# Performance work log

Hardware: AMD Instinct MI355X
Metric: run time of the kernel (lower is better)

The kernel has to match this reference:

```python
import jax, jax.numpy as jnp
import numpy as np
from jax import lax

N, R, W, H = 256, 32, 8, 6       # batch, n_rooms, room width/height
MX, MY = 72, 72                  # map grid
EMB = 6                          # room embedding width
CIN = 10 + EMB                   # conv input channels


def _boundaries(m):
    # m: [R, W, H] binary room masks -> [R, 4, W, H] (left, right, up, down edges)
    left = jnp.concatenate([m[:, :1, :], jnp.clip(m[:, 1:, :] - m[:, :-1, :], 0)], axis=1)
    right = jnp.concatenate([jnp.clip(m[:, :-1, :] - m[:, 1:, :], 0), m[:, -1:, :]], axis=1)
    up = jnp.concatenate([m[:, :, :1], jnp.clip(m[:, :, 1:] - m[:, :, :-1], 0)], axis=2)
    down = jnp.concatenate([jnp.clip(m[:, :, :-1] - m[:, :, 1:], 0), m[:, :, -1:]], axis=2)
    return jnp.stack([left, right, up, down], axis=1)


def setup_inputs() -> dict:
    key = jax.random.key(0)
    ks = jax.random.split(key, 12)
    room_map = (jax.random.uniform(ks[0], (R, W, H)) < 0.7).astype(jnp.float32)
    room_map = room_map.at[:, 0, 0].set(1.0)  # guarantee nonempty rooms
    doors = (jax.random.uniform(ks[1], (R, 4, W, H)) < 0.15).astype(jnp.float32) * room_map[:, None]
    room_tensor = jnp.concatenate([room_map[:, None], doors, _boundaries(room_map)], axis=1)  # [R,9,W,H]
    px = jax.random.randint(ks[2], (N, R), 0, MX - W)
    py = jax.random.randint(ks[3], (N, R), 0, MY - H)
    room_positions = jnp.stack([px, py], axis=-1).astype(jnp.int32)  # [N,R,2]

    def rn(k, shape, fan_in):
        return jax.random.normal(k, shape, jnp.float32) / np.float32(np.sqrt(fan_in))

    inp = dict(room_positions=room_positions, room_tensor=room_tensor)
    inp['room_embedding'] = jax.random.normal(ks[4], (R, EMB), jnp.float32)
    inp['w_conv1'] = rn(ks[5], (64, CIN, 5, 5), CIN * 25); inp['b_conv1'] = jnp.zeros((64,), jnp.float32)
    inp['w_conv2'] = rn(ks[6], (64, 64, 3, 3), 64 * 9);    inp['b_conv2'] = jnp.zeros((64,), jnp.float32)
    inp['w_conv3'] = rn(ks[7], (64, 64, 3, 3), 64 * 9);    inp['b_conv3'] = jnp.zeros((64,), jnp.float32)
    inp['w_room1'] = rn(ks[8], (128, 64), 64);   inp['b_room1'] = jnp.zeros((128,), jnp.float32)
    inp['w_room2'] = rn(ks[9], (128, 128), 128); inp['b_room2'] = jnp.zeros((128,), jnp.float32)
    inp['w_fc1'] = rn(ks[10], (256, 128), 128);  inp['b_fc1'] = jnp.zeros((256,), jnp.float32)
    inp['w_fc2'] = rn(ks[11], (256, 256), 256);  inp['b_fc2'] = jnp.zeros((256,), jnp.float32)
    return inp


def _conv2d_relu(x, w, b):
    pad = w.shape[-1] // 2
    y = lax.conv_general_dilated(x, w, (1, 1), [(pad, pad), (pad, pad)],
                                 dimension_numbers=('NCHW', 'OIHW', 'NCHW'))
    return jax.nn.relu(y + b[None, :, None, None])


def _forward(room_positions, room_tensor, room_embedding,
             w_conv1, b_conv1, w_conv2, b_conv2, w_conv3, b_conv3,
             w_room1, b_room1, w_room2, b_room2, w_fc1, b_fc1, w_fc2, b_fc2):
    room_map = room_tensor[:, 0]                      # [R,W,H]
    px = room_positions[..., 0]                       # [N,R]
    py = room_positions[..., 1]
    # ---- encode_map: scatter-add all rooms into grid ----
    bidx = jnp.arange(N)[:, None, None, None, None]
    cidx = jnp.arange(9)[None, None, :, None, None]
    ix = px[:, :, None, None, None] + jnp.arange(W)[None, None, None, :, None]   # [N,R,1,W,1]
    iy = py[:, :, None, None, None] + jnp.arange(H)[None, None, None, None, :]   # [N,R,1,1,H]
    map9 = jnp.zeros((N, 9, MX, MY), jnp.float32).at[bidx, cidx, ix, iy].add(room_tensor[None])
    eidx = jnp.arange(EMB)[None, None, :, None, None]
    evals = room_embedding[:, :, None, None] * room_map[:, None, :, :]           # [R,EMB,W,H]
    embg = jnp.zeros((N, EMB, MX, MY), jnp.float32).at[bidx, eidx, ix, iy].add(evals[None])
    X = jnp.concatenate([map9, jnp.ones((N, 1, MX, MY), jnp.float32), embg], axis=1)  # [N,16,MX,MY]
    # ---- map convs ----
    X = _conv2d_relu(X, w_conv1, b_conv1)
    X = _conv2d_relu(X, w_conv2, b_conv2)
    X = _conv2d_relu(X, w_conv3, b_conv3)
    # ---- decode_map: gather room tiles, masked mean per room ----
    Xt = jnp.transpose(X, (0, 2, 3, 1))                                          # [N,MX,MY,C]
    g = Xt[jnp.arange(N)[:, None, None, None],
           px[:, :, None, None] + jnp.arange(W)[None, None, :, None],
           py[:, :, None, None] + jnp.arange(H)[None, None, None, :]]            # [N,R,W,H,C]
    g = g * room_map[None, :, :, :, None]
    room_feat = g.sum(axis=(2, 3)) / room_map.sum(axis=(1, 2))[None, :, None]    # [N,R,C]
    X = jnp.transpose(room_feat, (0, 2, 1))                                      # [N,C,R]
    # ---- 1x1 conv1d room layers ----
    X = jax.nn.relu(jnp.einsum('ncr,oc->nor', X, w_room1) + b_room1[None, :, None])
    X = jax.nn.relu(jnp.einsum('ncr,oc->nor', X, w_room2) + b_room2[None, :, None])
    # ---- fc head: sum over rooms, MLP ----
    X = X.sum(axis=2)                                                            # [N,128]
    X = jax.nn.relu(X @ w_fc1.T + b_fc1)
    return X @ w_fc2.T + b_fc2                                                   # [N,256]


def reference(room_positions, room_tensor, room_embedding,
              w_conv1, b_conv1, w_conv2, b_conv2, w_conv3, b_conv3,
              w_room1, b_room1, w_room2, b_room2, w_fc1, b_fc1, w_fc2, b_fc2):
    return _forward(room_positions, room_tensor, room_embedding,
                    w_conv1, b_conv1, w_conv2, b_conv2, w_conv3, b_conv3,
                    w_room1, b_room1, w_room2, b_room2, w_fc1, b_fc1, w_fc2, b_fc2)
```

## Files before the change

### kernel.cpp

```cpp
#include <hip/hip_runtime.h>
#include <hip/hip_bf16.h>
#include <cstddef>

#define NB 256
#define RR 32
#define WW 8
#define HH 6
#define MXY 72
#define EMB 6
#define CIN1 16

typedef __bf16 bf16x8 __attribute__((ext_vector_type(8)));
typedef float floatx4 __attribute__((ext_vector_type(4)));

static const size_t B_W1F  = 0;
static const size_t B_W2F  = 57344;
static const size_t B_W3F  = 131072;
static const size_t B_RAUX = 204800;
static const size_t B_RINV = 205056;
static const size_t B_HEAD = 205312;
static const size_t F_WR1T = 0;
static const size_t F_WR2T = 8192;
static const size_t F_F1T  = 24576;
static const size_t F_F2T  = 57344;
static const size_t B_FEAT = 696832;
static const size_t B_CHUNK = 2793984;
static const size_t PERN_BYTES = 165888;

__device__ inline short f2b(float f) {
    unsigned u = __builtin_bit_cast(unsigned, f);
    unsigned r = (u + 0x7fffu + ((u >> 16) & 1u)) >> 16;
    return (short)r;
}

__global__ void prep_weights(const float* __restrict__ w1, const float* __restrict__ w2,
                             const float* __restrict__ w3, const float* __restrict__ wr1,
                             const float* __restrict__ wr2, const float* __restrict__ wf1,
                             const float* __restrict__ wf2, char* __restrict__ ws)
{
    short* W1F = (short*)(ws + B_W1F);
    short* W2F = (short*)(ws + B_W2F);
    short* W3F = (short*)(ws + B_W3F);
    float* HEAD = (float*)(ws + B_HEAD);

    int idx = blockIdx.x * 256 + threadIdx.x;
    if (idx < 28672) {
        int j = idx & 7, lane = (idx >> 3) & 63, nt = (idx >> 9) & 3, kk = idx >> 11;
        int k = kk * 32 + (lane >> 4) * 8 + j;
        int oc = nt * 16 + (lane & 15);
        int tap = k >> 4, ci = k & 15;
        float v = (tap < 25) ? w1[(oc * 16 + ci) * 25 + tap] : 0.f;
        W1F[idx] = f2b(v);
        return;
    }
    idx -= 28672;
    if (idx < 36864) {
        int j = idx & 7, lane = (idx >> 3) & 63, nt = (idx >> 9) & 3, kk = idx >> 11;
        int k = kk * 32 + (lane >> 4) * 8 + j;
        int oc = nt * 16 + (lane & 15);
        int tap = k >> 6, ci = k & 63;
        W2F[idx] = f2b(w2[(oc * 64 + ci) * 9 + tap]);
        return;
    }
    idx -= 36864;
    if (idx < 36864) {
        int j = idx & 7, lane = (idx >> 3) & 63, nt = (idx >> 9) & 3, kk = idx >> 11;
        int k = kk * 32 + (lane >> 4) * 8 + j;
        int oc = nt * 16 + (lane & 15);
        int tap = k >> 6, ci = k & 63;
        W3F[idx] = f2b(w3[(oc * 64 + ci) * 9 + tap]);
        return;
    }
    idx -= 36864;
    if (idx < 8192)  { int o = idx & 127, c = idx >> 7; HEAD[F_WR1T + idx] = wr1[o * 64 + c]; return; }
    idx -= 8192;
    if (idx < 16384) { int o = idx & 127, c = idx >> 7; HEAD[F_WR2T + idx] = wr2[o * 128 + c]; return; }
    idx -= 16384;
    if (idx < 32768) { int o = idx & 255, c = idx >> 8; HEAD[F_F1T + idx] = wf1[o * 128 + c]; return; }
    idx -= 32768;
    if (idx < 65536) { int o = idx & 255, c = idx >> 8; HEAD[F_F2T + idx] = wf2[o * 256 + c]; return; }
}

__global__ void prep_rooms(const float* __restrict__ rt, char* __restrict__ ws)
{
    int r = threadIdx.x;
    if (r >= RR) return;
    unsigned long long m = 0ull;
    int cnt = 0;
    for (int j = 0; j < WW * HH; ++j)
        if (rt[r * 9 * 48 + j] != 0.f) { m |= (1ull << j); ++cnt; }
    ((unsigned long long*)(ws + B_RAUX))[r] = m;
    ((float*)(ws + B_RINV))[r] = 1.f / (float)cnt;
}

__global__ __launch_bounds__(256) void build_x(const int* __restrict__ pos,
                                               const float* __restrict__ rt,
                                               const float* __restrict__ emb,
                                               short* __restrict__ X, int n0)
{
    const int nl = blockIdx.y;
    const int n = n0 + nl;
    const int p = blockIdx.x * 256 + threadIdx.x;

    __shared__ int s_px[RR], s_py[RR];
    __shared__ float s_emb[RR * EMB];
    if (threadIdx.x < RR) {
        s_px[threadIdx.x] = pos[(n * RR + threadIdx.x) * 2 + 0];
        s_py[threadIdx.x] = pos[(n * RR + threadIdx.x) * 2 + 1];
    }
    for (int i = threadIdx.x; i < RR * EMB; i += 256) s_emb[i] = emb[i];
    __syncthreads();
    if (p >= MXY * MXY) return;

    const int gx = p / MXY, gy = p - (p / MXY) * MXY;

    float acc[16];
#pragma unroll
    for (int c = 0; c < 16; ++c) acc[c] = 0.f;
    acc[9] = 1.f;

    for (int r = 0; r < RR; ++r) {
        int w = gx - s_px[r], h = gy - s_py[r];
        if ((unsigned)w < (unsigned)WW && (unsigned)h < (unsigned)HH) {
            int j = w * HH + h;
            const float* rr = rt + r * 9 * 48;
#pragma unroll
            for (int c = 0; c < 9; ++c) acc[c] += rr[c * 48 + j];
            float m = rr[j];
#pragma unroll
            for (int e = 0; e < EMB; ++e) acc[10 + e] += s_emb[r * EMB + e] * m;
        }
    }

    short o[16];
#pragma unroll
    for (int c = 0; c < 16; ++c) o[c] = f2b(acc[c]);
    short* dst = X + ((size_t)nl * (MXY * MXY) + p) * CIN1;
    *reinterpret_cast<uint4*>(dst) = *reinterpret_cast<uint4*>(o);
    *reinterpret_cast<uint4*>(dst + 8) = *reinterpret_cast<uint4*>(o + 8);
}

__global__ __launch_bounds__(256, 5) void fused_conv(const short* __restrict__ X,
    const short* __restrict__ W1F, const short* __restrict__ W2F,
    const short* __restrict__ W3F, const float* __restrict__ bc1,
    const float* __restrict__ bc2, const float* __restrict__ bc3,
    const int* __restrict__ pos, const unsigned long long* __restrict__ rmask,
    float* __restrict__ feat, int n0)
{
    __shared__ __align__(16) short s_Y1[120 * 72];
    __shared__ __align__(16) short s_u[80 * 72];
    __shared__ float s_feat[64];

    const int tid = threadIdx.x;
    const int lane = tid & 63;
    const int wv = tid >> 6;
    const int ml = lane & 15;
    const int q = lane >> 4;
    const int room = blockIdx.x;
    const int nl = blockIdx.y;
    const int n = n0 + nl;

    const int px = pos[(n * RR + room) * 2 + 0];
    const int py = pos[(n * RR + room) * 2 + 1];

    bf16x8 Bb[2][4];
    auto load_k = [&](const short* wF, int kk, bf16x8* dst) {
        const short* src = wF + (size_t)kk * 2048;
#pragma unroll
        for (int j2 = 0; j2 < 4; ++j2)
            dst[j2] = *reinterpret_cast<const bf16x8*>(src + (j2 * 64 + lane) * 8);
    };
    load_k(W1F, 0, Bb[0]);

    const short* Xn = X + (size_t)nl * (MXY * MXY) * CIN1;
    for (int i = tid; i < 448; i += 256) {
        int half = i & 1, pix = i >> 1;
        int row = pix / 14, col = pix - row * 14;
        int gx = px - 4 + row, gy = py - 4 + col;
        uint4 v = make_uint4(0u, 0u, 0u, 0u);
        if ((unsigned)gx < (unsigned)MXY && (unsigned)gy < (unsigned)MXY)
            v = *reinterpret_cast<const uint4*>(Xn + ((size_t)gx * MXY + gy) * CIN1 + half * 8);
        *reinterpret_cast<uint4*>(&s_u[pix * 24 + half * 8]) = v;
    }
    __syncthreads();

    floatx4 acc[2][4];

    {
        int prow[2], pcol[2];
#pragma unroll
        for (int i = 0; i < 2; ++i) {
            int p = wv * 32 + i * 16 + ml;
            if (p > 119) p = 119;
            prow[i] = p / 10; pcol[i] = p - prow[i] * 10;
        }
#pragma unroll
        for (int i = 0; i < 2; ++i)
#pragma unroll
            for (int j2 = 0; j2 < 4; ++j2) acc[i][j2] = (floatx4){0.f, 0.f, 0.f, 0.f};

#pragma unroll
        for (int kk = 0; kk < 13; ++kk) {
            if (kk < 12) load_k(W1F, kk + 1, Bb[(kk + 1) & 1]);
            else         load_k(W2F, 0, Bb[1]);
            int tap = kk * 2 + (q >> 1);
            if (tap > 24) tap = 24;
            int chb = (q & 1) * 8;
            int dx = tap / 5, dy = tap - dx * 5;
#pragma unroll
            for (int i = 0; i < 2; ++i) {
                bf16x8 A = *reinterpret_cast<const bf16x8*>(
                    &s_u[((prow[i] + dx) * 14 + (pcol[i] + dy)) * 24 + chb]);
#pragma unroll
                for (int j2 = 0; j2 < 4; ++j2)
                    acc[i][j2] = __builtin_amdgcn_mfma_f32_16x16x32_bf16(
                        A, Bb[kk & 1][j2], acc[i][j2], 0, 0, 0);
            }
        }
        float b4[4];
#pragma unroll
        for (int j2 = 0; j2 < 4; ++j2) b4[j2] = bc1[j2 * 16 + ml];
#pragma unroll
        for (int i = 0; i < 2; ++i)
#pragma unroll
            for (int r = 0; r < 4; ++r) {
                int p = wv * 32 + i * 16 + q * 4 + r;
                if (p < 120) {
#pragma unroll
                    for (int j2 = 0; j2 < 4; ++j2)
                        s_Y1[p * 72 + j2 * 16 + ml] = f2b(fmaxf(acc[i][j2][r] + b4[j2], 0.f));
                }
            }
    }
    __syncthreads();

    {
        int prow[2], pcol[2];
        {
            int p0 = wv * 16 + ml;
            prow[0] = p0 >> 3; pcol[0] = p0 & 7;
            int p1 = 64 + ml;
            prow[1] = p1 >> 3; pcol[1] = p1 & 7;
        }
#pragma unroll
        for (int i = 0; i < 2; ++i)
#pragma unroll
            for (int j2 = 0; j2 < 4; ++j2) acc[i][j2] = (floatx4){0.f, 0.f, 0.f, 0.f};

#pragma unroll
        for (int kk = 0; kk < 18; ++kk) {
            if (kk < 17) load_k(W2F, kk + 1, Bb[kk & 1]);
            else         load_k(W3F, 0, Bb[1]);
            int tap = kk >> 1;
            int chb = (kk & 1) * 32 + q * 8;
            int dx = tap / 3, dy = tap - dx * 3;
            bf16x8 A = *reinterpret_cast<const bf16x8*>(
                &s_Y1[((prow[0] + dx) * 10 + (pcol[0] + dy)) * 72 + chb]);
#pragma unroll
            for (int j2 = 0; j2 < 4; ++j2)
                acc[0][j2] = __builtin_amdgcn_mfma_f32_16x16x32_bf16(
                    A, Bb[(kk + 1) & 1][j2], acc[0][j2], 0, 0, 0);
            if (wv == 0) {
                bf16x8 A1 = *reinterpret_cast<const bf16x8*>(
                    &s_Y1[((prow[1] + dx) * 10 + (pcol[1] + dy)) * 72 + chb]);
#pragma unroll
                for (int j2 = 0; j2 < 4; ++j2)
                    acc[1][j2] = __builtin_amdgcn_mfma_f32_16x16x32_bf16(
                        A1, Bb[(kk + 1) & 1][j2], acc[1][j2], 0, 0, 0);
            }
        }
        float b4[4];
#pragma unroll
        for (int j2 = 0; j2 < 4; ++j2) b4[j2] = bc2[j2 * 16 + ml];
#pragma unroll
        for (int r = 0; r < 4; ++r) {
            int p = wv * 16 + q * 4 + r;
#pragma unroll
            for (int j2 = 0; j2 < 4; ++j2)
                s_u[p * 72 + j2 * 16 + ml] = f2b(fmaxf(acc[0][j2][r] + b4[j2], 0.f));
        }
        if (wv == 0) {
#pragma unroll
            for (int r = 0; r < 4; ++r) {
                int p = 64 + q * 4 + r;
#pragma unroll
                for (int j2 = 0; j2 < 4; ++j2)
                    s_u[p * 72 + j2 * 16 + ml] = f2b(fmaxf(acc[1][j2][r] + b4[j2], 0.f));
            }
        }
        if (tid < 64) s_feat[tid] = 0.f;
    }
    __syncthreads();

    if (wv < 3) {
        int p0 = wv * 16 + ml;
        int row = p0 / 6, col = p0 - row * 6;
#pragma unroll
        for (int j2 = 0; j2 < 4; ++j2) acc[0][j2] = (floatx4){0.f, 0.f, 0.f, 0.f};

#pragma unroll
        for (int kk = 0; kk < 18; ++kk) {
            if (kk < 17) load_k(W3F, kk + 1, Bb[kk & 1]);
            int tap = kk >> 1;
            int chb = (kk & 1) * 32 + q * 8;
            int dx = tap / 3, dy = tap - dx * 3;
            bf16x8 A = *reinterpret_cast<const bf16x8*>(
                &s_u[((row + dx) * 8 + (col + dy)) * 72 + chb]);
#pragma unroll
            for (int j2 = 0; j2 < 4; ++j2)
                acc[0][j2] = __builtin_amdgcn_mfma_f32_16x16x32_bf16(
                    A, Bb[(kk + 1) & 1][j2], acc[0][j2], 0, 0, 0);
        }
        float b4[4];
#pragma unroll
        for (int j2 = 0; j2 < 4; ++j2) b4[j2] = bc3[j2 * 16 + ml];
        float part[4] = {0.f, 0.f, 0.f, 0.f};
        const unsigned long long mk = rmask[room];
#pragma unroll
        for (int r = 0; r < 4; ++r) {
            int p = wv * 16 + q * 4 + r;
            if ((mk >> p) & 1ull) {
#pragma unroll
                for (int j2 = 0; j2 < 4; ++j2)
                    part[j2] += fmaxf(acc[0][j2][r] + b4[j2], 0.f);
            }
        }
#pragma unroll
        for (int j2 = 0; j2 < 4; ++j2) {
            part[j2] += __shfl_xor(part[j2], 16);
            part[j2] += __shfl_xor(part[j2], 32);
        }
        if (q == 0) {
#pragma unroll
            for (int j2 = 0; j2 < 4; ++j2)
                atomicAdd(&s_feat[j2 * 16 + ml], part[j2]);
        }
    }
    __syncthreads();
    if (tid < 64)
        feat[((size_t)n * RR + room) * 64 + tid] = s_feat[tid];
}

__global__ __launch_bounds__(256) void mlp_head(const float* __restrict__ feat,
                                                const float* __restrict__ HEAD,
                                                const float* __restrict__ rinv,
                                                const float* __restrict__ b1,
                                                const float* __restrict__ b2,
                                                const float* __restrict__ bf1,
                                                const float* __restrict__ bf2,
                                                float* __restrict__ outp)
{
    __shared__ __align__(16) float s_feat[RR * 64];
    __shared__ __align__(16) float s_h1[RR * 128];
    __shared__ __align__(16) float s_s[2 * 128];
    __shared__ __align__(16) float s_sf[128];
    __shared__ __align__(16) float s_t1[256];

    const int n = blockIdx.x;
    const int tid = threadIdx.x;
    const float* W1t = HEAD + F_WR1T;
    const float* W2t = HEAD + F_WR2T;
    const float* F1t = HEAD + F_F1T;
    const float* F2t = HEAD + F_F2T;

    for (int i = tid; i < RR * 64; i += 256)
        s_feat[i] = feat[(size_t)n * RR * 64 + i] * rinv[i >> 6];
    __syncthreads();

    const int o = tid & 127;
    const int rh = tid >> 7;

    float acc[16];
#pragma unroll
    for (int r = 0; r < 16; ++r) acc[r] = b1[o];
    for (int c4 = 0; c4 < 16; ++c4) {
        float w0 = W1t[(c4 * 4 + 0) * 128 + o];
        float w1 = W1t[(c4 * 4 + 1) * 128 + o];
        float w2 = W1t[(c4 * 4 + 2) * 128 + o];
        float w3 = W1t[(c4 * 4 + 3) * 128 + o];
#pragma unroll
        for (int r = 0; r < 16; ++r) {
            float4 f = *reinterpret_cast<const float4*>(&s_feat[(rh * 16 + r) * 64 + c4 * 4]);
            acc[r] += f.x * w0 + f.y * w1 + f.z * w2 + f.w * w3;
        }
    }
#pragma unroll
    for (int r = 0; r < 16; ++r) s_h1[(rh * 16 + r) * 128 + o] = fmaxf(acc[r], 0.f);
    __syncthreads();

#pragma unroll
    for (int r = 0; r < 16; ++r) acc[r] = b2[o];
    for (int c4 = 0; c4 < 32; ++c4) {
        float w0 = W2t[(c4 * 4 + 0) * 128 + o];
        float w1 = W2t[(c4 * 4 + 1) * 128 + o];
        float w2 = W2t[(c4 * 4 + 2) * 128 + o];
        float w3 = W2t[(c4 * 4 + 3) * 128 + o];
#pragma unroll
        for (int r = 0; r < 16; ++r) {
            float4 f = *reinterpret_cast<const float4*>(&s_h1[(rh * 16 + r) * 128 + c4 * 4]);
            acc[r] += f.x * w0 + f.y * w1 + f.z * w2 + f.w * w3;
        }
    }
    float ps = 0.f;
#pragma unroll
    for (int r = 0; r < 16; ++r) ps += fmaxf(acc[r], 0.f);
    s_s[rh * 128 + o] = ps;
    __syncthreads();
    if (tid < 128) s_sf[tid] = s_s[tid] + s_s[128 + tid];
    __syncthreads();

    {
        float a = bf1[tid];
        for (int c4 = 0; c4 < 32; ++c4) {
            float4 f = *reinterpret_cast<const float4*>(&s_sf[c4 * 4]);
            a += f.x * F1t[(c4 * 4 + 0) * 256 + tid];
            a += f.y * F1t[(c4 * 4 + 1) * 256 + tid];
            a += f.z * F1t[(c4 * 4 + 2) * 256 + tid];
            a += f.w * F1t[(c4 * 4 + 3) * 256 + tid];
        }
        s_t1[tid] = fmaxf(a, 0.f);
    }
    __syncthreads();

    {
        float a = bf2[tid];
        for (int c4 = 0; c4 < 64; ++c4) {
            float4 f = *reinterpret_cast<const float4*>(&s_t1[c4 * 4]);
            a += f.x * F2t[(c4 * 4 + 0) * 256 + tid];
            a += f.y * F2t[(c4 * 4 + 1) * 256 + tid];
            a += f.z * F2t[(c4 * 4 + 2) * 256 + tid];
            a += f.w * F2t[(c4 * 4 + 3) * 256 + tid];
        }
        outp[(size_t)n * 256 + tid] = a;
    }
}

extern "C" void kernel_launch(void* const* d_in, const int* in_sizes, int n_in,
                              void* d_out, int out_size, void* d_ws, size_t ws_size,
                              hipStream_t stream)
{
    const int* pos = (const int*)d_in[0];
    const float* rt = (const float*)d_in[1];
    const float* emb = (const float*)d_in[2];
    const float* w1 = (const float*)d_in[3];
    const float* bc1 = (const float*)d_in[4];
    const float* w2 = (const float*)d_in[5];
    const float* bc2 = (const float*)d_in[6];
    const float* w3 = (const float*)d_in[7];
    const float* bc3 = (const float*)d_in[8];
    const float* wr1 = (const float*)d_in[9];
    const float* br1 = (const float*)d_in[10];
    const float* wr2 = (const float*)d_in[11];
    const float* br2 = (const float*)d_in[12];
    const float* wf1 = (const float*)d_in[13];
    const float* bf1 = (const float*)d_in[14];
    const float* wf2 = (const float*)d_in[15];
    const float* bf2 = (const float*)d_in[16];
    float* out = (float*)d_out;
    char* ws = (char*)d_ws;

    prep_weights<<<880, 256, 0, stream>>>(w1, w2, w3, wr1, wr2, wf1, wf2, ws);
    prep_rooms<<<1, 64, 0, stream>>>(rt, ws);

    int nc = 16;
    const int cands[4] = {256, 128, 64, 32};
    for (int k = 0; k < 4; ++k) {
        size_t need = B_CHUNK + (size_t)cands[k] * PERN_BYTES;
        if (need <= ws_size) { nc = cands[k]; break; }
    }

    short* W1F = (short*)(ws + B_W1F);
    short* W2F = (short*)(ws + B_W2F);
    short* W3F = (short*)(ws + B_W3F);
    const unsigned long long* RMASK = (const unsigned long long*)(ws + B_RAUX);
    const float* RINV = (const float*)(ws + B_RINV);
    float* HEAD = (float*)(ws + B_HEAD);
    float* FEAT = (float*)(ws + B_FEAT);
    short* Xc = (short*)(ws + B_CHUNK);

    for (int n0 = 0; n0 < NB; n0 += nc) {
        build_x<<<dim3(21, nc), 256, 0, stream>>>(pos, rt, emb, Xc, n0);
        fused_conv<<<dim3(RR, nc), 256, 0, stream>>>(Xc, W1F, W2F, W3F,
                                                     bc1, bc2, bc3, pos, RMASK, FEAT, n0);
    }

    mlp_head<<<NB, 256, 0, stream>>>(FEAT, HEAD, RINV, br1, br2, bf1, bf2, out);
}
```

Before: 325.3 us.

## Stream conv weights into LDS via async DMA double buffer, rebalance conv2 tail

Weight fragments for all three convs are no longer loaded straight into registers. Each workgroup now copies them from global memory into a double-buffered LDS stage with global_load_lds, one phase of two K-blocks per barrier, and the waves read the B fragments from LDS. The leftover 16-pixel tile of conv2 is spread across all four waves, one output slice per wave, instead of being done by wave 0 alone. Weights are permuted on the host so the conv1 and conv2 outputs can be packed into uint2 LDS stores, and s_setprio is placed around the MFMA bursts. The cost is extra LDS use and more barriers, and launch bounds drop from 5 to 3 waves per SIMD, which lowers occupancy.

Result: faster. 313.3 us (-3.7%).

```diff
diff --git a/kernel.cpp b/kernel.cpp
--- a/kernel.cpp
+++ b/kernel.cpp
@@ -58,7 +58,8 @@
         int j = idx & 7, lane = (idx >> 3) & 63, nt = (idx >> 9) & 3, kk = idx >> 11;
         int k = kk * 32 + (lane >> 4) * 8 + j;
         int oc = nt * 16 + (lane & 15);
-        int tap = k >> 6, ci = k & 63;
+        int tap = k >> 6, cp = k & 63;
+        int ci = (cp >> 2) + (cp & 3) * 16;
         W2F[idx] = f2b(w2[(oc * 64 + ci) * 9 + tap]);
         return;
     }
@@ -67,7 +68,8 @@
         int j = idx & 7, lane = (idx >> 3) & 63, nt = (idx >> 9) & 3, kk = idx >> 11;
         int k = kk * 32 + (lane >> 4) * 8 + j;
         int oc = nt * 16 + (lane & 15);
-        int tap = k >> 6, ci = k & 63;
+        int tap = k >> 6, cp = k & 63;
+        int ci = (cp >> 2) + (cp & 3) * 16;
         W3F[idx] = f2b(w3[(oc * 64 + ci) * 9 + tap]);
         return;
     }
@@ -140,15 +142,15 @@
     *reinterpret_cast<uint4*>(dst + 8) = *reinterpret_cast<uint4*>(o + 8);
 }
 
-__global__ __launch_bounds__(256, 5) void fused_conv(const short* __restrict__ X,
-    const short* __restrict__ W1F, const short* __restrict__ W2F,
-    const short* __restrict__ W3F, const float* __restrict__ bc1,
+__global__ __launch_bounds__(256, 3) void fused_conv(const short* __restrict__ X,
+    const short* __restrict__ wAll, const float* __restrict__ bc1,
     const float* __restrict__ bc2, const float* __restrict__ bc3,
     const int* __restrict__ pos, const unsigned long long* __restrict__ rmask,
     float* __restrict__ feat, int n0)
 {
     __shared__ __align__(16) short s_Y1[120 * 72];
     __shared__ __align__(16) short s_u[80 * 72];
+    __shared__ __align__(16) short s_B[2][4096];
     __shared__ float s_feat[64];
 
     const int tid = threadIdx.x;
@@ -163,14 +165,19 @@
     const int px = pos[(n * RR + room) * 2 + 0];
     const int py = pos[(n * RR + room) * 2 + 1];
 
-    bf16x8 Bb[2][4];
-    auto load_k = [&](const short* wF, int kk, bf16x8* dst) {
-        const short* src = wF + (size_t)kk * 2048;
-#pragma unroll
-        for (int j2 = 0; j2 < 4; ++j2)
-            dst[j2] = *reinterpret_cast<const bf16x8*>(src + (j2 * 64 + lane) * 8);
+    const char* wB = (const char*)wAll;
+    auto dma = [&](int ph) {
+        const char* src = wB + (size_t)ph * 8192 + wv * 2048 + lane * 16;
+        short* d0 = &s_B[ph & 1][wv * 1024];
+        __builtin_amdgcn_global_load_lds(
+            (const __attribute__((address_space(1))) unsigned int*)src,
+            (__attribute__((address_space(3))) unsigned int*)d0, 16, 0, 0);
+        __builtin_amdgcn_global_load_lds(
+            (const __attribute__((address_space(1))) unsigned int*)(src + 1024),
+            (__attribute__((address_space(3))) unsigned int*)(d0 + 512), 16, 0, 0);
     };
-    load_k(W1F, 0, Bb[0]);
+
+    dma(0);
 
     const short* Xn = X + (size_t)nl * (MXY * MXY) * CIN1;
     for (int i = tid; i < 448; i += 256) {
@@ -184,8 +191,6 @@
     }
     __syncthreads();
 
-    floatx4 acc[2][4];
-
     {
         int prow[2], pcol[2];
 #pragma unroll
@@ -194,149 +199,179 @@
             if (p > 119) p = 119;
             prow[i] = p / 10; pcol[i] = p - prow[i] * 10;
         }
-#pragma unroll
-        for (int i = 0; i < 2; ++i)
-#pragma unroll
-            for (int j2 = 0; j2 < 4; ++j2) acc[i][j2] = (floatx4){0.f, 0.f, 0.f, 0.f};
-
-#pragma unroll
-        for (int kk = 0; kk < 13; ++kk) {
-            if (kk < 12) load_k(W1F, kk + 1, Bb[(kk + 1) & 1]);
-            else         load_k(W2F, 0, Bb[1]);
-            int tap = kk * 2 + (q >> 1);
-            if (tap > 24) tap = 24;
-            int chb = (q & 1) * 8;
-            int dx = tap / 5, dy = tap - dx * 5;
-#pragma unroll
-            for (int i = 0; i < 2; ++i) {
-                bf16x8 A = *reinterpret_cast<const bf16x8*>(
-                    &s_u[((prow[i] + dx) * 14 + (pcol[i] + dy)) * 24 + chb]);
+        floatx4 acc1[2][4] = {};
+
+#pragma unroll
+        for (int t = 0; t < 7; ++t) {
+            dma(t + 1);
+            const short* sb = s_B[t & 1];
+#pragma unroll
+            for (int kb = 0; kb < 2; ++kb) {
+                const int kk = t * 2 + kb;
+                bf16x8 Bf[4];
 #pragma unroll
                 for (int j2 = 0; j2 < 4; ++j2)
-                    acc[i][j2] = __builtin_amdgcn_mfma_f32_16x16x32_bf16(
-                        A, Bb[kk & 1][j2], acc[i][j2], 0, 0, 0);
+                    Bf[j2] = *reinterpret_cast<const bf16x8*>(&sb[kb * 2048 + (j2 * 64 + lane) * 8]);
+                int tap = kk * 2 + (q >> 1);
+                if (tap > 24) tap = 24;
+                const int chb = (q & 1) * 8;
+                const int dx = tap / 5, dy = tap - (tap / 5) * 5;
+                __builtin_amdgcn_s_setprio(1);
+#pragma unroll
+                for (int i = 0; i < 2; ++i) {
+                    bf16x8 A = *reinterpret_cast<const bf16x8*>(
+                        &s_u[((prow[i] + dx) * 14 + (pcol[i] + dy)) * 24 + chb]);
+#pragma unroll
+                    for (int j2 = 0; j2 < 4; ++j2)
+                        acc1[i][j2] = __builtin_amdgcn_mfma_f32_16x16x32_bf16(
+                            A, Bf[j2], acc1[i][j2], 0, 0, 0);
+                }
+                __builtin_amdgcn_s_setprio(0);
             }
-        }
-        float b4[4];
-#pragma unroll
-        for (int j2 = 0; j2 < 4; ++j2) b4[j2] = bc1[j2 * 16 + ml];
-#pragma unroll
-        for (int i = 0; i < 2; ++i)
-#pragma unroll
-            for (int r = 0; r < 4; ++r) {
-                int p = wv * 32 + i * 16 + q * 4 + r;
-                if (p < 120) {
-#pragma unroll
-                    for (int j2 = 0; j2 < 4; ++j2)
-                        s_Y1[p * 72 + j2 * 16 + ml] = f2b(fmaxf(acc[i][j2][r] + b4[j2], 0.f));
-                }
+            if (t == 6) {
+                float b4[4];
+#pragma unroll
+                for (int j2 = 0; j2 < 4; ++j2) b4[j2] = bc1[j2 * 16 + ml];
+#pragma unroll
+                for (int i = 0; i < 2; ++i)
+#pragma unroll
+                    for (int r = 0; r < 4; ++r) {
+                        int p = wv * 32 + i * 16 + q * 4 + r;
+                        if (p < 120) {
+                            unsigned lo = (unsigned)(unsigned short)f2b(fmaxf(acc1[i][0][r] + b4[0], 0.f))
+                                        | ((unsigned)(unsigned short)f2b(fmaxf(acc1[i][1][r] + b4[1], 0.f)) << 16);
+                            unsigned hi = (unsigned)(unsigned short)f2b(fmaxf(acc1[i][2][r] + b4[2], 0.f))
+                                        | ((unsigned)(unsigned short)f2b(fmaxf(acc1[i][3][r] + b4[3], 0.f)) << 16);
+                            *reinterpret_cast<uint2*>(&s_Y1[p * 72 + ml * 4]) = make_uint2(lo, hi);
+                        }
+                    }
             }
-    }
-    __syncthreads();
+            __syncthreads();
+        }
+    }
 
     {
-        int prow[2], pcol[2];
+        int prowA, pcolA, prowB, pcolB;
+        {
+            int p0 = wv * 16 + ml; prowA = p0 >> 3; pcolA = p0 & 7;
+            int p1 = 64 + ml;      prowB = p1 >> 3; pcolB = p1 & 7;
+        }
+        floatx4 acc2[4] = {};
+        floatx4 acc2t = {};
+
+#pragma unroll
+        for (int t = 0; t < 9; ++t) {
+            dma(8 + t);
+            const short* sb = s_B[(7 + t) & 1];
+#pragma unroll
+            for (int kb = 0; kb < 2; ++kb) {
+                const int kk = t * 2 + kb;
+                bf16x8 Bf[4];
+#pragma unroll
+                for (int j2 = 0; j2 < 4; ++j2)
+                    Bf[j2] = *reinterpret_cast<const bf16x8*>(&sb[kb * 2048 + (j2 * 64 + lane) * 8]);
+                bf16x8 B4 = *reinterpret_cast<const bf16x8*>(&sb[kb * 2048 + (wv * 64 + lane) * 8]);
+                const int tap = kk >> 1;
+                const int chb = (kk & 1) * 32 + q * 8;
+                const int dx = tap / 3, dy = tap - (tap / 3) * 3;
+                bf16x8 A0 = *reinterpret_cast<const bf16x8*>(
+                    &s_Y1[((prowA + dx) * 10 + (pcolA + dy)) * 72 + chb]);
+                bf16x8 A4 = *reinterpret_cast<const bf16x8*>(
+                    &s_Y1[((prowB + dx) * 10 + (pcolB + dy)) * 72 + chb]);
+                __builtin_amdgcn_s_setprio(1);
+#pragma unroll
+                for (int j2 = 0; j2 < 4; ++j2)
+                    acc2[j2] = __builtin_amdgcn_mfma_f32_16x16x32_bf16(A0, Bf[j2], acc2[j2], 0, 0, 0);
+                acc2t = __builtin_amdgcn_mfma_f32_16x16x32_bf16(A4, B4, acc2t, 0, 0, 0);
+                __builtin_amdgcn_s_setprio(0);
+            }
+            if (t == 8) {
+                float b4[4];
+#pragma unroll
+                for (int j2 = 0; j2 < 4; ++j2) b4[j2] = bc2[j2 * 16 + ml];
+#pragma unroll
+                for (int r = 0; r < 4; ++r) {
+                    int p = wv * 16 + q * 4 + r;
+                    unsigned lo = (unsigned)(unsigned short)f2b(fmaxf(acc2[0][r] + b4[0], 0.f))
+                                | ((unsigned)(unsigned short)f2b(fmaxf(acc2[1][r] + b4[1], 0.f)) << 16);
+                    unsigned hi = (unsigned)(unsigned short)f2b(fmaxf(acc2[2][r] + b4[2], 0.f))
+                                | ((unsigned)(unsigned short)f2b(fmaxf(acc2[3][r] + b4[3], 0.f)) << 16);
+                    *reinterpret_cast<uint2*>(&s_u[p * 72 + ml * 4]) = make_uint2(lo, hi);
+                }
+                float bt = bc2[wv * 16 + ml];
+#pragma unroll
+                for (int r = 0; r < 4; ++r) {
+                    int p = 64 + q * 4 + r;
+                    s_u[p * 72 + ml * 4 + wv] = f2b(fmaxf(acc2t[r] + bt, 0.f));
+                }
+                if (tid < 64) s_feat[tid] = 0.f;
+            }
+            __syncthreads();
+        }
+    }
+
+    {
+        int prow3, pcol3;
         {
             int p0 = wv * 16 + ml;
-            prow[0] = p0 >> 3; pcol[0] = p0 & 7;
-            int p1 = 64 + ml;
-            prow[1] = p1 >> 3; pcol[1] = p1 & 7;
-        }
-#pragma unroll
-        for (int i = 0; i < 2; ++i)
-#pragma unroll
-            for (int j2 = 0; j2 < 4; ++j2) acc[i][j2] = (floatx4){0.f, 0.f, 0.f, 0.f};
-
-#pragma unroll
-        for (int kk = 0; kk < 18; ++kk) {
-            if (kk < 17) load_k(W2F, kk + 1, Bb[kk & 1]);
-            else         load_k(W3F, 0, Bb[1]);
-            int tap = kk >> 1;
-            int chb = (kk & 1) * 32 + q * 8;
-            int dx = tap / 3, dy = tap - dx * 3;
-            bf16x8 A = *reinterpret_cast<const bf16x8*>(
-                &s_Y1[((prow[0] + dx) * 10 + (pcol[0] + dy)) * 72 + chb]);
-#pragma unroll
-            for (int j2 = 0; j2 < 4; ++j2)
-                acc[0][j2] = __builtin_amdgcn_mfma_f32_16x16x32_bf16(
-                    A, Bb[(kk + 1) & 1][j2], acc[0][j2], 0, 0, 0);
-            if (wv == 0) {
-                bf16x8 A1 = *reinterpret_cast<const bf16x8*>(
-                    &s_Y1[((prow[1] + dx) * 10 + (pcol[1] + dy)) * 72 + chb]);
-#pragma unroll
-                for (int j2 = 0; j2 < 4; ++j2)
-                    acc[1][j2] = __builtin_amdgcn_mfma_f32_16x16x32_bf16(
-                        A1, Bb[(kk + 1) & 1][j2], acc[1][j2], 0, 0, 0);
+            prow3 = p0 / 6; pcol3 = p0 - prow3 * 6;
+        }
+        floatx4 acc3[4] = {};
+
+#pragma unroll
+        for (int t = 0; t < 9; ++t) {
+            if (t < 8) dma(17 + t);
+            const short* sb = s_B[(16 + t) & 1];
+            if (wv < 3) {
+#pragma unroll
+                for (int kb = 0; kb < 2; ++kb) {
+                    const int kk = t * 2 + kb;
+                    bf16x8 Bf[4];
+#pragma unroll
+                    for (int j2 = 0; j2 < 4; ++j2)
+                        Bf[j2] = *reinterpret_cast<const bf16x8*>(&sb[kb * 2048 + (j2 * 64 + lane) * 8]);
+                    const int tap = kk >> 1;
+                    const int chb = (kk & 1) * 32 + q * 8;
+                    const int dx = tap / 3, dy = tap - (tap / 3) * 3;
+                    bf16x8 A = *reinterpret_cast<const bf16x8*>(
+                        &s_u[((prow3 + dx) * 8 + (pcol3 + dy)) * 72 + chb]);
+                    __builtin_amdgcn_s_setprio(1);
+#pragma unroll
+                    for (int j2 = 0; j2 < 4; ++j2)
+                        acc3[j2] = __builtin_amdgcn_mfma_f32_16x16x32_bf16(A, Bf[j2], acc3[j2], 0, 0, 0);
+                    __builtin_amdgcn_s_setprio(0);
+                }
             }
-        }
-        float b4[4];
-#pragma unroll
-        for (int j2 = 0; j2 < 4; ++j2) b4[j2] = bc2[j2 * 16 + ml];
-#pragma unroll
-        for (int r = 0; r < 4; ++r) {
-            int p = wv * 16 + q * 4 + r;
-#pragma unroll
-            for (int j2 = 0; j2 < 4; ++j2)
-                s_u[p * 72 + j2 * 16 + ml] = f2b(fmaxf(acc[0][j2][r] + b4[j2], 0.f));
-        }
-        if (wv == 0) {
-#pragma unroll
-            for (int r = 0; r < 4; ++r) {
-                int p = 64 + q * 4 + r;
-#pragma unroll
-                for (int j2 = 0; j2 < 4; ++j2)
-                    s_u[p * 72 + j2 * 16 + ml] = f2b(fmaxf(acc[1][j2][r] + b4[j2], 0.f));
+            if (t == 8 && wv < 3) {
+                float b4[4];
+#pragma unroll
+                for (int j2 = 0; j2 < 4; ++j2) b4[j2] = bc3[j2 * 16 + ml];
+                float part[4] = {0.f, 0.f, 0.f, 0.f};
+                const unsigned long long mk = rmask[room];
+#pragma unroll
+                for (int r = 0; r < 4; ++r) {
+                    int p = wv * 16 + q * 4 + r;
+                    if ((mk >> p) & 1ull) {
+#pragma unroll
+                        for (int j2 = 0; j2 < 4; ++j2)
+                            part[j2] += fmaxf(acc3[j2][r] + b4[j2], 0.f);
+                    }
+                }
+#pragma unroll
+                for (int j2 = 0; j2 < 4; ++j2) {
+                    part[j2] += __shfl_xor(part[j2], 16);
+                    part[j2] += __shfl_xor(part[j2], 32);
+                }
+                if (q == 0) {
+#pragma unroll
+                    for (int j2 = 0; j2 < 4; ++j2)
+                        atomicAdd(&s_feat[j2 * 16 + ml], part[j2]);
+                }
             }
-        }
-        if (tid < 64) s_feat[tid] = 0.f;
-    }
-    __syncthreads();
-
-    if (wv < 3) {
-        int p0 = wv * 16 + ml;
-        int row = p0 / 6, col = p0 - row * 6;
-#pragma unroll
-        for (int j2 = 0; j2 < 4; ++j2) acc[0][j2] = (floatx4){0.f, 0.f, 0.f, 0.f};
-
-#pragma unroll
-        for (int kk = 0; kk < 18; ++kk) {
-            if (kk < 17) load_k(W3F, kk + 1, Bb[kk & 1]);
-            int tap = kk >> 1;
-            int chb = (kk & 1) * 32 + q * 8;
-            int dx = tap / 3, dy = tap - dx * 3;
-            bf16x8 A = *reinterpret_cast<const bf16x8*>(
-                &s_u[((row + dx) * 8 + (col + dy)) * 72 + chb]);
-#pragma unroll
-            for (int j2 = 0; j2 < 4; ++j2)
-                acc[0][j2] = __builtin_amdgcn_mfma_f32_16x16x32_bf16(
-                    A, Bb[(kk + 1) & 1][j2], acc[0][j2], 0, 0, 0);
-        }
-        float b4[4];
-#pragma unroll
-        for (int j2 = 0; j2 < 4; ++j2) b4[j2] = bc3[j2 * 16 + ml];
-        float part[4] = {0.f, 0.f, 0.f, 0.f};
-        const unsigned long long mk = rmask[room];
-#pragma unroll
-        for (int r = 0; r < 4; ++r) {
-            int p = wv * 16 + q * 4 + r;
-            if ((mk >> p) & 1ull) {
-#pragma unroll
-                for (int j2 = 0; j2 < 4; ++j2)
-                    part[j2] += fmaxf(acc[0][j2][r] + b4[j2], 0.f);
-            }
-        }
-#pragma unroll
-        for (int j2 = 0; j2 < 4; ++j2) {
-            part[j2] += __shfl_xor(part[j2], 16);
-            part[j2] += __shfl_xor(part[j2], 32);
-        }
-        if (q == 0) {
-#pragma unroll
-            for (int j2 = 0; j2 < 4; ++j2)
-                atomicAdd(&s_feat[j2 * 16 + ml], part[j2]);
-        }
-    }
-    __syncthreads();
+            __syncthreads();
+        }
+    }
+
     if (tid < 64)
         feat[((size_t)n * RR + room) * 64 + tid] = s_feat[tid];
 }
@@ -469,9 +504,7 @@
         if (need <= ws_size) { nc = cands[k]; break; }
     }
 
-    short* W1F = (short*)(ws + B_W1F);
-    short* W2F = (short*)(ws + B_W2F);
-    short* W3F = (short*)(ws + B_W3F);
+    const short* WALL = (const short*)(ws + B_W1F);
     const unsigned long long* RMASK = (const unsigned long long*)(ws + B_RAUX);
     const float* RINV = (const float*)(ws + B_RINV);
     float* HEAD = (float*)(ws + B_HEAD);
@@ -480,8 +513,8 @@
 
     for (int n0 = 0; n0 < NB; n0 += nc) {
         build_x<<<dim3(21, nc), 256, 0, stream>>>(pos, rt, emb, Xc, n0);
-        fused_conv<<<dim3(RR, nc), 256, 0, stream>>>(Xc, W1F, W2F, W3F,
-                                                     bc1, bc2, bc3, pos, RMASK, FEAT, n0);
+        fused_conv<<<dim3(RR, nc), 256, 0, stream>>>(Xc, WALL, bc1, bc2, bc3,
+                                                     pos, RMASK, FEAT, n0);
     }
 
     mlp_head<<<NB, 256, 0, stream>>>(FEAT, HEAD, RINV, br1, br2, bf1, bf2, out);
```
